# Kernel tuning notes

Measured on AMD Instinct MI355X. Metric: run time of the kernel, lower is better.

The kernel has to match this reference:

```python
import jax, jax.numpy as jnp
import numpy as np

D_MODEL = 1024
NUM_HEADS = 16
D_K = D_MODEL // NUM_HEADS


def setup_inputs() -> dict:
    key = jax.random.key(0)
    ks = jax.random.split(key, 11)
    B, S = 4, 2048
    s = 1.0 / np.sqrt(D_MODEL)
    return {
        "query": jax.random.normal(ks[0], (B, S, D_MODEL), jnp.float32),
        "key": jax.random.normal(ks[1], (B, S, D_MODEL), jnp.float32),
        "value": jax.random.normal(ks[2], (B, S, D_MODEL), jnp.float32),
        "Wq": jax.random.normal(ks[3], (D_MODEL, D_MODEL), jnp.float32) * s,
        "bq": jnp.zeros((D_MODEL,), jnp.float32),
        "Wk": jax.random.normal(ks[4], (D_MODEL, D_MODEL), jnp.float32) * s,
        "bk": jnp.zeros((D_MODEL,), jnp.float32),
        "Wv": jax.random.normal(ks[5], (D_MODEL, D_MODEL), jnp.float32) * s,
        "bv": jnp.zeros((D_MODEL,), jnp.float32),
        "Wo": jax.random.normal(ks[6], (D_MODEL, D_MODEL), jnp.float32) * s,
        "bo": jnp.zeros((D_MODEL,), jnp.float32),
    }


def reference(query, key, value, Wq, bq, Wk, bk, Wv, bv, Wo, bo):
    B, Sq, _ = query.shape
    Sk = key.shape[1]
    # linear projections (torch Linear: x @ W.T + b)
    q = query @ Wq.T + bq
    k = key @ Wk.T + bk
    v = value @ Wv.T + bv
    # [B, H, S, d_k]
    q = q.reshape(B, Sq, NUM_HEADS, D_K).transpose(0, 2, 1, 3)
    k = k.reshape(B, Sk, NUM_HEADS, D_K).transpose(0, 2, 1, 3)
    v = v.reshape(B, Sk, NUM_HEADS, D_K).transpose(0, 2, 1, 3)
    scores = jnp.einsum("bhqd,bhkd->bhqk", q, k) / jnp.sqrt(jnp.float32(D_K)).astype(q.dtype)
    attn = jax.nn.softmax(scores, axis=-1)
    out = jnp.einsum("bhqk,bhkd->bhqd", attn, v)
    out = out.transpose(0, 2, 1, 3).reshape(B, Sq, D_MODEL)
    return out @ Wo.T + bo
```

## Files before the change

### kernel.cpp

```cpp
#include <hip/hip_runtime.h>
#include <hip/hip_bf16.h>
#include <cstdint>
#include <cstddef>

typedef __attribute__((ext_vector_type(8))) short bf16x8;
typedef __attribute__((ext_vector_type(4))) short bf16x4;
typedef __attribute__((ext_vector_type(4))) float f32x4;
typedef __attribute__((ext_vector_type(2))) unsigned int u32x2;

#define NH 16
#define DK 64
#define SEQ 2048
#define DM 1024
#define QSCALE 0.18033688011112042f

__device__ __forceinline__ short f2bf(float f) {
    union { float f; unsigned u; } x; x.f = f;
    unsigned r = x.u + 0x7fffu + ((x.u >> 16) & 1u);
    return (short)(r >> 16);
}

__device__ __forceinline__ unsigned pk2(float a, float b) {
    union { float f; unsigned u; } x, y; x.f = a; y.f = b;
    return __builtin_amdgcn_perm(y.u + 0x8000u, x.u + 0x8000u, 0x07060302u);
}

__device__ __forceinline__ void glds16(const short* g, short* l) {
    __builtin_amdgcn_global_load_lds((const __attribute__((address_space(1))) unsigned int*)g,
                                     (__attribute__((address_space(3))) unsigned int*)l, 16, 0, 0);
}

__global__ __launch_bounds__(256)
void cvt_all(const float* __restrict__ xq, const float* __restrict__ xk, const float* __restrict__ xv,
             const float* __restrict__ Wq, const float* __restrict__ Wk,
             const float* __restrict__ Wv, const float* __restrict__ Wo,
             short* __restrict__ xb0, short* __restrict__ xb1, short* __restrict__ xb2,
             short* __restrict__ Wb)
{
    const int bid = blockIdx.x;
    const float* src;
    short* dst;
    float sc = 1.0f;
    int i;
    if (bid < 12288) {
        int z = bid >> 12;
        src = (z == 0) ? xq : (z == 1) ? xk : xv;
        dst = (z == 0) ? xb0 : (z == 1) ? xb1 : xb2;
        i = (bid & 4095) * 2048 + threadIdx.x * 8;
    } else {
        int wb = bid - 12288;
        int z = wb >> 9;
        src = (z == 0) ? Wq : (z == 1) ? Wk : (z == 2) ? Wv : Wo;
        dst = Wb + (size_t)z * DM * DM;
        sc = (z == 0) ? QSCALE : 1.0f;
        i = (wb & 511) * 2048 + threadIdx.x * 8;
    }
    float4 a = *(const float4*)&src[i];
    float4 b = *(const float4*)&src[i + 4];
    bf16x8 o = { f2bf(a.x * sc), f2bf(a.y * sc), f2bf(a.z * sc), f2bf(a.w * sc),
                 f2bf(b.x * sc), f2bf(b.y * sc), f2bf(b.z * sc), f2bf(b.w * sc) };
    *(bf16x8*)&dst[i] = o;
}

__global__ __launch_bounds__(256)
void cvt_x(const float* __restrict__ src, short* __restrict__ dst)
{
    int i = (blockIdx.x * 256 + threadIdx.x) * 8;
    float4 a = *(const float4*)&src[i];
    float4 b = *(const float4*)&src[i + 4];
    bf16x8 o = { f2bf(a.x), f2bf(a.y), f2bf(a.z), f2bf(a.w),
                 f2bf(b.x), f2bf(b.y), f2bf(b.z), f2bf(b.w) };
    *(bf16x8*)&dst[i] = o;
}

__global__ __launch_bounds__(256)
void cvt_w(const float* __restrict__ Wq, const float* __restrict__ Wk,
           const float* __restrict__ Wv, const float* __restrict__ Wo,
           short* __restrict__ dst)
{
    int z = blockIdx.y;
    const float* s = (z == 0) ? Wq : (z == 1) ? Wk : (z == 2) ? Wv : Wo;
    float sc = (z == 0) ? QSCALE : 1.0f;
    int i = (blockIdx.x * 256 + threadIdx.x) * 8;
    float4 a = *(const float4*)&s[i];
    float4 b = *(const float4*)&s[i + 4];
    bf16x8 o = { f2bf(a.x * sc), f2bf(a.y * sc), f2bf(a.z * sc), f2bf(a.w * sc),
                 f2bf(b.x * sc), f2bf(b.y * sc), f2bf(b.z * sc), f2bf(b.w * sc) };
    *(bf16x8*)&dst[(size_t)z * DM * DM + i] = o;
}

#define GEMM_CORE(P0, OFF0, P1, OFF1)                                                      \
    __shared__ short As[128 * 32];                                                         \
    __shared__ short Bs[128 * 32];                                                         \
    f32x4 acc[4][4] = {};                                                                  \
    const int t = threadIdx.x;                                                             \
    const int lane = t & 63;                                                               \
    const int w = t >> 6;                                                                  \
    const int wm = (w >> 1) * 64, wn = (w & 1) * 64;                                       \
    const int l15 = lane & 15, quad = lane >> 4;                                           \
    const int g0 = t, g1 = 256 + t;                                                        \
    const int r0 = g0 >> 2, r1 = g1 >> 2;                                                  \
    const int c0 = ((g0 & 3) ^ ((r0 >> 1) & 3)) * 8;                                       \
    const int c1 = ((g1 & 3) ^ ((r1 >> 1) & 3)) * 8;                                       \
    for (int k0 = 0; k0 < DM; k0 += 32) {                                                  \
        glds16(&P0[(size_t)(OFF0 + r0) * DM + k0 + c0], &As[g0 * 8]);                      \
        glds16(&P0[(size_t)(OFF0 + r1) * DM + k0 + c1], &As[g1 * 8]);                      \
        glds16(&P1[(size_t)(OFF1 + r0) * DM + k0 + c0], &Bs[g0 * 8]);                      \
        glds16(&P1[(size_t)(OFF1 + r1) * DM + k0 + c1], &Bs[g1 * 8]);                      \
        __syncthreads();                                                                   \
        bf16x8 a[4], b[4];                                                                 \
        _Pragma("unroll")                                                                  \
        for (int i = 0; i < 4; i++) {                                                      \
            int row = wm + i * 16 + l15;                                                   \
            a[i] = *(bf16x8*)&As[row * 32 + (quad ^ ((row >> 1) & 3)) * 8];                \
        }                                                                                  \
        _Pragma("unroll")                                                                  \
        for (int j = 0; j < 4; j++) {                                                      \
            int row = wn + j * 16 + l15;                                                   \
            b[j] = *(bf16x8*)&Bs[row * 32 + (quad ^ ((row >> 1) & 3)) * 8];                \
        }                                                                                  \
        _Pragma("unroll")                                                                  \
        for (int i = 0; i < 4; i++)                                                        \
            _Pragma("unroll")                                                              \
            for (int j = 0; j < 4; j++)                                                    \
                acc[i][j] = __builtin_amdgcn_mfma_f32_16x16x32_bf16(a[i], b[j], acc[i][j], 0, 0, 0); \
        __syncthreads();                                                                   \
    }

__global__ __launch_bounds__(256)
void gemm_qkv(const short* __restrict__ x0, const short* __restrict__ x1, const short* __restrict__ x2,
              const short* __restrict__ Wball,
              const float* __restrict__ bq, const float* __restrict__ bk, const float* __restrict__ bv,
              short* __restrict__ qws, short* __restrict__ kws, short* __restrict__ vws,
              int zoff)
{
    const int z = blockIdx.z + zoff;
    const short* X = (z == 0) ? x0 : (z == 1) ? x1 : x2;
    const short* W = Wball + (size_t)z * DM * DM;
    const float* bias = (z == 0) ? bq : (z == 1) ? bk : bv;
    const float bscale = (z == 0) ? QSCALE : 1.0f;

    const int tn = blockIdx.x * 128;
    const int tm = blockIdx.y * 128;
    const int vm = (z == 2);

    const short* P0 = vm ? X : W;   const int OFF0 = vm ? tm : tn;
    const short* P1 = vm ? W : X;   const int OFF1 = vm ? tn : tm;
    GEMM_CORE(P0, OFF0, P1, OFF1)

    if (vm) {
#pragma unroll
        for (int j = 0; j < 4; j++) {
            int n = tn + wn + j * 16 + l15;
            float bn = bias[n];
            int h = n >> 6, d = n & 63;
#pragma unroll
            for (int i = 0; i < 4; i++) {
                int m0 = tm + wm + i * 16 + quad * 4;
                int bb = m0 >> 11, s0 = m0 & (SEQ - 1);
                u32x2 u = { pk2(acc[i][j][0] + bn, acc[i][j][1] + bn),
                            pk2(acc[i][j][2] + bn, acc[i][j][3] + bn) };
                *(u32x2*)&vws[((size_t)((bb * NH + h) * 64 + d)) * SEQ + s0] = u;
            }
        }
    } else {
        short* dst = (z == 0) ? qws : kws;
#pragma unroll
        for (int i = 0; i < 4; i++) {
            int n0 = tn + wm + i * 16 + quad * 4;
            float4 b4 = *(const float4*)&bias[n0];
            int h = n0 >> 6, d0 = n0 & 63;
#pragma unroll
            for (int j = 0; j < 4; j++) {
                int m = tm + wn + j * 16 + l15;
                int bb = m >> 11, s = m & (SEQ - 1);
                u32x2 u = { pk2(acc[i][j][0] + b4.x * bscale, acc[i][j][1] + b4.y * bscale),
                            pk2(acc[i][j][2] + b4.z * bscale, acc[i][j][3] + b4.w * bscale) };
                *(u32x2*)&dst[((((size_t)(bb * NH + h)) * SEQ + s) << 6) + d0] = u;
            }
        }
    }
}

__global__ __launch_bounds__(256)
void out_proj(const short* __restrict__ A, const short* __restrict__ W,
              const float* __restrict__ bias, float* __restrict__ out)
{
    const int tn = blockIdx.x * 128;
    const int tm = blockIdx.y * 128;
    GEMM_CORE(A, tm, W, tn)

#pragma unroll
    for (int j = 0; j < 4; j++) {
        int n = tn + wn + j * 16 + l15;
        float bn = bias[n];
#pragma unroll
        for (int i = 0; i < 4; i++)
#pragma unroll
            for (int r = 0; r < 4; r++) {
                int m = tm + wm + i * 16 + quad * 4 + r;
                out[(size_t)m * DM + n] = acc[i][j][r] + bn;
            }
    }
}

__global__ __launch_bounds__(256, 4)
void attn(const short* __restrict__ Q, const short* __restrict__ K, const short* __restrict__ V,
          short* __restrict__ O)
{
    const int bh = blockIdx.x;
    const int b = bh >> 4, h = bh & 15;
    const int qt = blockIdx.y;
    const size_t base = (size_t)bh * SEQ * DK;
    const size_t vbase = (size_t)bh * DK * SEQ;

    const int t = threadIdx.x;
    const int lane = t & 63;
    const int w = t >> 6;
    const int l15 = lane & 15, quad = lane >> 4;
    const int l7 = l15 & 7;

    __shared__ short Kt[64 * 64];
    __shared__ short Vt[80 * 64];
    __shared__ short Pt[4][32 * 64];

    if (t < 128) {
        int row = 64 + (t >> 3);
        short val = (row == 64) ? (short)0x3F80 : (short)0;
        bf16x8 fill = { val, val, val, val, val, val, val, val };
        *(bf16x8*)&Vt[row * 64 + (t & 7) * 8] = fill;
    }

    bf16x8 qb[2][2];
    const int qrow0 = qt * 128 + w * 32;
#pragma unroll
    for (int nq = 0; nq < 2; nq++)
#pragma unroll
        for (int kd = 0; kd < 2; kd++)
            qb[nq][kd] = *(const bf16x8*)&Q[base + (size_t)(qrow0 + nq * 16 + l15) * DK + kd * 32 + quad * 8];

    f32x4 oT[5][2] = {};

    const int sr = t >> 2;
    const int sc = (t & 3) * 16;
    const int sg0 = (((t & 3) * 2) ^ (sr & 7)) * 8;
    const int sg1 = (((t & 3) * 2 + 1) ^ (sr & 7)) * 8;

    bf16x8 kr0 = *(const bf16x8*)&K[base + (size_t)sr * DK + sc];
    bf16x8 kr1 = *(const bf16x8*)&K[base + (size_t)sr * DK + sc + 8];
    bf16x8 vr0 = *(const bf16x8*)&V[vbase + (size_t)sr * SEQ + sc];
    bf16x8 vr1 = *(const bf16x8*)&V[vbase + (size_t)sr * SEQ + sc + 8];

    for (int kt = 0; kt < SEQ / 64; kt++) {
        *(bf16x8*)&Kt[sr * 64 + sg0] = kr0;
        *(bf16x8*)&Kt[sr * 64 + sg1] = kr1;
        *(bf16x8*)&Vt[sr * 64 + sg0] = vr0;
        *(bf16x8*)&Vt[sr * 64 + sg1] = vr1;
        __syncthreads();

        if (kt < SEQ / 64 - 1) {
            const short* kg = &K[base + (size_t)((kt + 1) * 64 + sr) * DK + sc];
            const short* vg = &V[vbase + (size_t)sr * SEQ + (kt + 1) * 64 + sc];
            kr0 = *(const bf16x8*)&kg[0];
            kr1 = *(const bf16x8*)&kg[8];
            vr0 = *(const bf16x8*)&vg[0];
            vr1 = *(const bf16x8*)&vg[8];
        }

        f32x4 st[4][2] = {};
#pragma unroll
        for (int kd = 0; kd < 2; kd++) {
#pragma unroll
            for (int mf = 0; mf < 4; mf++) {
                bf16x8 ka = *(bf16x8*)&Kt[(mf * 16 + l15) * 64 + ((kd * 4 + quad) ^ l7) * 8];
#pragma unroll
                for (int nq = 0; nq < 2; nq++)
                    st[mf][nq] = __builtin_amdgcn_mfma_f32_16x16x32_bf16(ka, qb[nq][kd], st[mf][nq], 0, 0, 0);
            }
        }

#pragma unroll
        for (int nq = 0; nq < 2; nq++) {
            const int prow = (nq * 16 + l15) * 64;
#pragma unroll
            for (int mf = 0; mf < 4; mf++) {
#pragma unroll
                for (int r = 0; r < 4; r++)
                    st[mf][nq][r] = __builtin_amdgcn_exp2f(st[mf][nq][r]);
                u32x2 u = { pk2(st[mf][nq][0], st[mf][nq][1]),
                            pk2(st[mf][nq][2], st[mf][nq][3]) };
                *(u32x2*)&Pt[w][prow + (((mf * 2 + (quad >> 1)) ^ l7) * 8) + (quad & 1) * 4] = u;
            }
        }

#pragma unroll
        for (int kk = 0; kk < 2; kk++) {
            bf16x8 pb[2];
#pragma unroll
            for (int nq = 0; nq < 2; nq++)
                pb[nq] = *(bf16x8*)&Pt[w][(nq * 16 + l15) * 64 + ((kk * 4 + quad) ^ l7) * 8];
#pragma unroll
            for (int mfd = 0; mfd < 5; mfd++) {
                bf16x8 va = *(bf16x8*)&Vt[(mfd * 16 + l15) * 64 + ((kk * 4 + quad) ^ l7) * 8];
#pragma unroll
                for (int nq = 0; nq < 2; nq++)
                    oT[mfd][nq] = __builtin_amdgcn_mfma_f32_16x16x32_bf16(va, pb[nq], oT[mfd][nq], 0, 0, 0);
            }
        }
        __syncthreads();
    }

#pragma unroll
    for (int nq = 0; nq < 2; nq++) {
        float lsum = __shfl(oT[4][nq][0], l15);
        float inv = 1.0f / lsum;
        int s = qrow0 + nq * 16 + l15;
#pragma unroll
        for (int mfd = 0; mfd < 4; mfd++) {
            u32x2 u = { pk2(oT[mfd][nq][0] * inv, oT[mfd][nq][1] * inv),
                        pk2(oT[mfd][nq][2] * inv, oT[mfd][nq][3] * inv) };
            *(u32x2*)&O[((size_t)(b * SEQ + s)) * DM + h * 64 + mfd * 16 + quad * 4] = u;
        }
    }
}

extern "C" void kernel_launch(void* const* d_in, const int* in_sizes, int n_in,
                              void* d_out, int out_size, void* d_ws, size_t ws_size,
                              hipStream_t stream)
{
    const float* q_in = (const float*)d_in[0];
    const float* k_in = (const float*)d_in[1];
    const float* v_in = (const float*)d_in[2];
    const float* Wq = (const float*)d_in[3];
    const float* bq = (const float*)d_in[4];
    const float* Wk = (const float*)d_in[5];
    const float* bk = (const float*)d_in[6];
    const float* Wv = (const float*)d_in[7];
    const float* bv = (const float*)d_in[8];
    const float* Wo = (const float*)d_in[9];
    const float* bo = (const float*)d_in[10];
    float* out = (float*)d_out;

    char* ws = (char*)d_ws;
    const size_t MB = (size_t)1024 * 1024;
    short* qws = (short*)d_out;
    short* kws = (short*)d_out + (size_t)8 * MB;
    const size_t NW = (size_t)DM * DM;

    if (ws_size >= 88 * MB) {
        short* xb0 = (short*)(ws);
        short* xb1 = (short*)(ws + 16 * MB);
        short* xb2 = (short*)(ws + 32 * MB);
        short* vws = (short*)(ws + 48 * MB);
        short* ows = (short*)(ws + 64 * MB);
        short* Wb  = (short*)(ws + 80 * MB);

        cvt_all<<<dim3(14336), 256, 0, stream>>>(q_in, k_in, v_in, Wq, Wk, Wv, Wo, xb0, xb1, xb2, Wb);
        gemm_qkv<<<dim3(8, 64, 3), 256, 0, stream>>>(xb0, xb1, xb2, Wb, bq, bk, bv, qws, kws, vws, 0);
        attn<<<dim3(64, 16), 256, 0, stream>>>(qws, kws, vws, ows);
        out_proj<<<dim3(8, 64), 256, 0, stream>>>(ows, Wb + 3 * NW, bo, out);
    } else {
        short* xb  = (short*)(ws);
        short* vws = (short*)(ws + 16 * MB);
        short* ows = (short*)(ws + 32 * MB);
        short* Wb  = (short*)(ws + 48 * MB);
        const int xblocks = (4 * SEQ * DM) / 2048;

        cvt_w<<<dim3((int)(NW / 2048), 4), 256, 0, stream>>>(Wq, Wk, Wv, Wo, Wb);
        cvt_x<<<dim3(xblocks), 256, 0, stream>>>(q_in, xb);
        gemm_qkv<<<dim3(8, 64, 1), 256, 0, stream>>>(xb, xb, xb, Wb, bq, bk, bv, qws, kws, vws, 0);
        cvt_x<<<dim3(xblocks), 256, 0, stream>>>(k_in, xb);
        gemm_qkv<<<dim3(8, 64, 1), 256, 0, stream>>>(xb, xb, xb, Wb, bq, bk, bv, qws, kws, vws, 1);
        cvt_x<<<dim3(xblocks), 256, 0, stream>>>(v_in, xb);
        gemm_qkv<<<dim3(8, 64, 1), 256, 0, stream>>>(xb, xb, xb, Wb, bq, bk, bv, qws, kws, vws, 2);
        attn<<<dim3(64, 16), 256, 0, stream>>>(qws, kws, vws, ows);
        out_proj<<<dim3(8, 64), 256, 0, stream>>>(ows, Wb + 3 * NW, bo, out);
    }
}
```

Baseline: 343.8 us.

## Double-buffer attention K/V via direct LDS loads and keep P in registers

The attention kernel now loads K/V tiles with global_load_lds into double-buffered shared memory, which removes the register staging and the second barrier per tile. The P matrix no longer makes a round trip through LDS: exp'd scores are packed with v_cvt_pk_bf16_f32 and rearranged across lanes with v_permlane32_swap. The V projection epilogue permutes the sequence positions within 32-element groups so they match that register layout. The grid order is swapped so that blocks sharing a head run together, for better K/V cache reuse. In exchange it relies on gfx950-specific instructions, uses more LDS per block, and needs the V layout permutation to match exactly.

Result: no change. 345.8 us (+0.6%).

```diff
diff --git a/kernel.cpp b/kernel.cpp
--- a/kernel.cpp
+++ b/kernel.cpp
@@ -7,6 +7,7 @@
 typedef __attribute__((ext_vector_type(4))) short bf16x4;
 typedef __attribute__((ext_vector_type(4))) float f32x4;
 typedef __attribute__((ext_vector_type(2))) unsigned int u32x2;
+typedef __attribute__((ext_vector_type(4))) unsigned int u32x4;
 
 #define NH 16
 #define DK 64
@@ -23,6 +24,16 @@
 __device__ __forceinline__ unsigned pk2(float a, float b) {
     union { float f; unsigned u; } x, y; x.f = a; y.f = b;
     return __builtin_amdgcn_perm(y.u + 0x8000u, x.u + 0x8000u, 0x07060302u);
+}
+
+__device__ __forceinline__ unsigned cvtpk(float a, float b) {
+    unsigned r;
+    asm("v_cvt_pk_bf16_f32 %0, %1, %2" : "=v"(r) : "v"(a), "v"(b));
+    return r;
+}
+
+__device__ __forceinline__ void plswap32(unsigned& a, unsigned& b) {
+    asm("v_permlane32_swap_b32 %0, %1" : "+v"(a), "+v"(b));
 }
 
 __device__ __forceinline__ void glds16(const short* g, short* l) {
@@ -158,9 +169,12 @@
             for (int i = 0; i < 4; i++) {
                 int m0 = tm + wm + i * 16 + quad * 4;
                 int bb = m0 >> 11, s0 = m0 & (SEQ - 1);
+                int g = (s0 >> 2) & 7;
+                int gp = (g & 4) | ((g & 1) << 1) | ((g >> 1) & 1);
+                int sp = (s0 & ~31) | (gp << 2);
                 u32x2 u = { pk2(acc[i][j][0] + bn, acc[i][j][1] + bn),
                             pk2(acc[i][j][2] + bn, acc[i][j][3] + bn) };
-                *(u32x2*)&vws[((size_t)((bb * NH + h) * 64 + d)) * SEQ + s0] = u;
+                *(u32x2*)&vws[((size_t)((bb * NH + h) * 64 + d)) * SEQ + sp] = u;
             }
         }
     } else {
@@ -208,9 +222,9 @@
 void attn(const short* __restrict__ Q, const short* __restrict__ K, const short* __restrict__ V,
           short* __restrict__ O)
 {
-    const int bh = blockIdx.x;
+    const int qt = blockIdx.x;
+    const int bh = blockIdx.y;
     const int b = bh >> 4, h = bh & 15;
-    const int qt = blockIdx.y;
     const size_t base = (size_t)bh * SEQ * DK;
     const size_t vbase = (size_t)bh * DK * SEQ;
 
@@ -220,16 +234,26 @@
     const int l15 = lane & 15, quad = lane >> 4;
     const int l7 = l15 & 7;
 
-    __shared__ short Kt[64 * 64];
-    __shared__ short Vt[80 * 64];
-    __shared__ short Pt[4][32 * 64];
-
-    if (t < 128) {
-        int row = 64 + (t >> 3);
+    __shared__ short Kt[2][64 * 64];
+    __shared__ short Vt[2][80 * 64];
+
+    {
+        int buf = t >> 7;
+        int row = 64 + ((t >> 3) & 15);
         short val = (row == 64) ? (short)0x3F80 : (short)0;
         bf16x8 fill = { val, val, val, val, val, val, val, val };
-        *(bf16x8*)&Vt[row * 64 + (t & 7) * 8] = fill;
-    }
+        *(bf16x8*)&Vt[buf][row * 64 + (t & 7) * 8] = fill;
+    }
+
+    const int sr = t >> 3, su = t & 7;
+    const int swz = (su ^ (sr & 7)) * 8;
+    const short* kp0 = &K[base + (size_t)sr * DK + swz];
+    const short* vp0 = &V[vbase + (size_t)sr * SEQ + swz];
+
+    glds16(kp0,               &Kt[0][sr * 64 + su * 8]);
+    glds16(kp0 + 32 * DK,     &Kt[0][(32 + sr) * 64 + su * 8]);
+    glds16(vp0,               &Vt[0][sr * 64 + su * 8]);
+    glds16(vp0 + 32 * SEQ,    &Vt[0][(32 + sr) * 64 + su * 8]);
 
     bf16x8 qb[2][2];
     const int qrow0 = qt * 128 + w * 32;
@@ -241,73 +265,59 @@
 
     f32x4 oT[5][2] = {};
 
-    const int sr = t >> 2;
-    const int sc = (t & 3) * 16;
-    const int sg0 = (((t & 3) * 2) ^ (sr & 7)) * 8;
-    const int sg1 = (((t & 3) * 2 + 1) ^ (sr & 7)) * 8;
-
-    bf16x8 kr0 = *(const bf16x8*)&K[base + (size_t)sr * DK + sc];
-    bf16x8 kr1 = *(const bf16x8*)&K[base + (size_t)sr * DK + sc + 8];
-    bf16x8 vr0 = *(const bf16x8*)&V[vbase + (size_t)sr * SEQ + sc];
-    bf16x8 vr1 = *(const bf16x8*)&V[vbase + (size_t)sr * SEQ + sc + 8];
-
     for (int kt = 0; kt < SEQ / 64; kt++) {
-        *(bf16x8*)&Kt[sr * 64 + sg0] = kr0;
-        *(bf16x8*)&Kt[sr * 64 + sg1] = kr1;
-        *(bf16x8*)&Vt[sr * 64 + sg0] = vr0;
-        *(bf16x8*)&Vt[sr * 64 + sg1] = vr1;
         __syncthreads();
-
+        const int cur = kt & 1;
         if (kt < SEQ / 64 - 1) {
-            const short* kg = &K[base + (size_t)((kt + 1) * 64 + sr) * DK + sc];
-            const short* vg = &V[vbase + (size_t)sr * SEQ + (kt + 1) * 64 + sc];
-            kr0 = *(const bf16x8*)&kg[0];
-            kr1 = *(const bf16x8*)&kg[8];
-            vr0 = *(const bf16x8*)&vg[0];
-            vr1 = *(const bf16x8*)&vg[8];
-        }
-
-        f32x4 st[4][2] = {};
-#pragma unroll
-        for (int kd = 0; kd < 2; kd++) {
-#pragma unroll
-            for (int mf = 0; mf < 4; mf++) {
-                bf16x8 ka = *(bf16x8*)&Kt[(mf * 16 + l15) * 64 + ((kd * 4 + quad) ^ l7) * 8];
-#pragma unroll
-                for (int nq = 0; nq < 2; nq++)
-                    st[mf][nq] = __builtin_amdgcn_mfma_f32_16x16x32_bf16(ka, qb[nq][kd], st[mf][nq], 0, 0, 0);
-            }
-        }
-
-#pragma unroll
-        for (int nq = 0; nq < 2; nq++) {
-            const int prow = (nq * 16 + l15) * 64;
-#pragma unroll
-            for (int mf = 0; mf < 4; mf++) {
-#pragma unroll
-                for (int r = 0; r < 4; r++)
-                    st[mf][nq][r] = __builtin_amdgcn_exp2f(st[mf][nq][r]);
-                u32x2 u = { pk2(st[mf][nq][0], st[mf][nq][1]),
-                            pk2(st[mf][nq][2], st[mf][nq][3]) };
-                *(u32x2*)&Pt[w][prow + (((mf * 2 + (quad >> 1)) ^ l7) * 8) + (quad & 1) * 4] = u;
-            }
-        }
-
-#pragma unroll
-        for (int kk = 0; kk < 2; kk++) {
+            const int nxt = cur ^ 1;
+            const int kb = (kt + 1) * 64;
+            glds16(kp0 + (size_t)kb * DK,        &Kt[nxt][sr * 64 + su * 8]);
+            glds16(kp0 + (size_t)(kb + 32) * DK, &Kt[nxt][(32 + sr) * 64 + su * 8]);
+            glds16(vp0 + kb,                     &Vt[nxt][sr * 64 + su * 8]);
+            glds16(vp0 + kb + 32 * SEQ,          &Vt[nxt][(32 + sr) * 64 + su * 8]);
+        }
+
+#pragma unroll
+        for (int half = 0; half < 2; half++) {
+            f32x4 st[2][2] = {};
+#pragma unroll
+            for (int kd = 0; kd < 2; kd++) {
+#pragma unroll
+                for (int m2 = 0; m2 < 2; m2++) {
+                    const int mf = half * 2 + m2;
+                    bf16x8 ka = *(bf16x8*)&Kt[cur][(mf * 16 + l15) * 64 + ((kd * 4 + quad) ^ l7) * 8];
+#pragma unroll
+                    for (int nq = 0; nq < 2; nq++)
+                        st[m2][nq] = __builtin_amdgcn_mfma_f32_16x16x32_bf16(ka, qb[nq][kd], st[m2][nq], 0, 0, 0);
+                }
+            }
+
             bf16x8 pb[2];
 #pragma unroll
-            for (int nq = 0; nq < 2; nq++)
-                pb[nq] = *(bf16x8*)&Pt[w][(nq * 16 + l15) * 64 + ((kk * 4 + quad) ^ l7) * 8];
+            for (int nq = 0; nq < 2; nq++) {
+#pragma unroll
+                for (int m2 = 0; m2 < 2; m2++)
+#pragma unroll
+                    for (int r = 0; r < 4; r++)
+                        st[m2][nq][r] = __builtin_amdgcn_exp2f(st[m2][nq][r]);
+                unsigned W0 = cvtpk(st[0][nq][0], st[0][nq][1]);
+                unsigned W1 = cvtpk(st[0][nq][2], st[0][nq][3]);
+                unsigned W2 = cvtpk(st[1][nq][0], st[1][nq][1]);
+                unsigned W3 = cvtpk(st[1][nq][2], st[1][nq][3]);
+                plswap32(W0, W2);
+                plswap32(W1, W3);
+                u32x4 uu = { W0, W1, W2, W3 };
+                pb[nq] = *(bf16x8*)&uu;
+            }
+
 #pragma unroll
             for (int mfd = 0; mfd < 5; mfd++) {
-                bf16x8 va = *(bf16x8*)&Vt[(mfd * 16 + l15) * 64 + ((kk * 4 + quad) ^ l7) * 8];
+                bf16x8 va = *(bf16x8*)&Vt[cur][(mfd * 16 + l15) * 64 + ((half * 4 + quad) ^ l7) * 8];
 #pragma unroll
                 for (int nq = 0; nq < 2; nq++)
                     oT[mfd][nq] = __builtin_amdgcn_mfma_f32_16x16x32_bf16(va, pb[nq], oT[mfd][nq], 0, 0, 0);
             }
         }
-        __syncthreads();
     }
 
 #pragma unroll
@@ -317,8 +327,8 @@
         int s = qrow0 + nq * 16 + l15;
 #pragma unroll
         for (int mfd = 0; mfd < 4; mfd++) {
-            u32x2 u = { pk2(oT[mfd][nq][0] * inv, oT[mfd][nq][1] * inv),
-                        pk2(oT[mfd][nq][2] * inv, oT[mfd][nq][3] * inv) };
+            u32x2 u = { cvtpk(oT[mfd][nq][0] * inv, oT[mfd][nq][1] * inv),
+                        cvtpk(oT[mfd][nq][2] * inv, oT[mfd][nq][3] * inv) };
             *(u32x2*)&O[((size_t)(b * SEQ + s)) * DM + h * 64 + mfd * 16 + quad * 4] = u;
         }
     }
@@ -357,7 +367,7 @@
 
         cvt_all<<<dim3(14336), 256, 0, stream>>>(q_in, k_in, v_in, Wq, Wk, Wv, Wo, xb0, xb1, xb2, Wb);
         gemm_qkv<<<dim3(8, 64, 3), 256, 0, stream>>>(xb0, xb1, xb2, Wb, bq, bk, bv, qws, kws, vws, 0);
-        attn<<<dim3(64, 16), 256, 0, stream>>>(qws, kws, vws, ows);
+        attn<<<dim3(16, 64), 256, 0, stream>>>(qws, kws, vws, ows);
         out_proj<<<dim3(8, 64), 256, 0, stream>>>(ows, Wb + 3 * NW, bo, out);
     } else {
         short* xb  = (short*)(ws);
@@ -373,7 +383,7 @@
         gemm_qkv<<<dim3(8, 64, 1), 256, 0, stream>>>(xb, xb, xb, Wb, bq, bk, bv, qws, kws, vws, 1);
         cvt_x<<<dim3(xblocks), 256, 0, stream>>>(v_in, xb);
         gemm_qkv<<<dim3(8, 64, 1), 256, 0, stream>>>(xb, xb, xb, Wb, bq, bk, bv, qws, kws, vws, 2);
-        attn<<<dim3(64, 16), 256, 0, stream>>>(qws, kws, vws, ows);
+        attn<<<dim3(16, 64), 256, 0, stream>>>(qws, kws, vws, ows);
         out_proj<<<dim3(8, 64), 256, 0, stream>>>(ows, Wb + 3 * NW, bo, out);
     }
 }
```
